# Performance work log

Hardware: AMD Instinct MI355X
Metric: run time of the kernel (lower is better)

The kernel has to match this reference:

```python
import jax, jax.numpy as jnp
import numpy as np

B, T1, T2 = 16, 1024, 1024
K1D, K2D, V1D, V2D, A = 512, 512, 256, 256, 128


def setup_inputs() -> dict:
    key = jax.random.key(0)
    ks = jax.random.split(key, 10)
    inp = {
        "k1": jax.random.normal(ks[0], (B, T1, K1D), dtype=jnp.float32),
        "k2": jax.random.normal(ks[1], (B, T2, K2D), dtype=jnp.float32),
        "v1": jax.random.normal(ks[2], (B, T1, V1D), dtype=jnp.float32),
        "v2": jax.random.normal(ks[3], (B, T2, V2D), dtype=jnp.float32),
        # Linear params (torch nn.Linear: y = x @ W.T + b)
        "W1": jax.random.normal(ks[4], (A, K1D), dtype=jnp.float32) / np.sqrt(K1D),
        "b1": jnp.zeros((A,), dtype=jnp.float32),
        "W2": jax.random.normal(ks[5], (A, K2D), dtype=jnp.float32) / np.sqrt(K2D),
        "b2": jnp.zeros((A,), dtype=jnp.float32),
        # valid lengths in [T/2, T-1] so no softmax row is entirely -inf
        "k1_lengths": jax.random.randint(ks[6], (B,), T1 // 2, T1, dtype=jnp.int32),
        "k2_lengths": jax.random.randint(ks[7], (B,), T2 // 2, T2, dtype=jnp.int32),
    }
    return inp


def reference(k1, k2, v1, v2, W1, b1, W2, b2, k1_lengths, k2_lengths):
    # projections
    q1 = jnp.einsum("bti,ai->bta", k1, W1) + b1  # [B,T1,A]
    q2 = jnp.einsum("bti,ai->bta", k2, W2) + b2  # [B,T2,A]
    # co-attention score [B,T1,T2]
    score = jnp.einsum("bia,bja->bij", q1, q2)
    # faithful mask: torch code adds 1 for rows>=l1 and 1 for cols>=l2,
    # then masks where sum == 1  -> XOR of the two pad conditions.
    row_pad = jnp.arange(T1)[None, :, None] >= k1_lengths[:, None, None]  # [B,T1,1]
    col_pad = jnp.arange(T2)[None, None, :] >= k2_lengths[:, None, None]  # [B,1,T2]
    mask = jnp.logical_xor(row_pad, col_pad)
    score = jnp.where(mask, -jnp.inf, score)
    # dual softmaxes
    w1 = jax.nn.softmax(jnp.swapaxes(score, 1, 2), axis=-1)  # [B,T2,T1]
    w2 = jax.nn.softmax(score, axis=-1)                      # [B,T1,T2]
    o1 = jnp.einsum("bji,bid->bjd", w1, v1)  # [B,T2,V1D]
    o2 = jnp.einsum("bij,bjd->bid", w2, v2)  # [B,T1,V2D]
    # note: the torch module additionally slices w1/w2/score per sample to
    # (l2,l1)/(l1,l2) ragged views; with fixed shapes we return the full
    # tensors (the valid region matches; slicing is a zero-copy view in torch).
    return (o1, o2, w1, w2, score)
```

## Files before the change

kernel.cpp:

```cpp
#include <hip/hip_runtime.h>
#include <math.h>

namespace {
constexpr int TT   = 1024;
constexpr int AD   = 128;
constexpr int KDIM = 512;
constexpr int VDIM = 256;
constexpr int NB   = 16;
constexpr size_t T2T = (size_t)TT * TT;
constexpr size_t BT  = (size_t)NB * TT;
}

#define MASK_VAL (-1.0e30f)

typedef __bf16 bf16x8 __attribute__((ext_vector_type(8)));
typedef float  f32x4  __attribute__((ext_vector_type(4)));

__device__ __forceinline__ unsigned short bf16_rne(float x) {
    unsigned int u = __builtin_bit_cast(unsigned int, x);
    u += 0x7fffu + ((u >> 16) & 1u);
    return (unsigned short)(u >> 16);
}
__device__ __forceinline__ float bf16f(unsigned short h) {
    return __builtin_bit_cast(float, ((unsigned int)h) << 16);
}
__device__ __forceinline__ void split2(float x, unsigned short& h, unsigned short& l) {
    h = bf16_rne(x);
    l = bf16_rne(x - bf16f(h));
}

__global__ __launch_bounds__(256) void prep_vt_kernel(
    const float* __restrict__ v1, const float* __restrict__ v2,
    unsigned short* __restrict__ vth, unsigned short* __restrict__ vtl)
{
    const int b     = blockIdx.x;
    const int k0    = blockIdx.y * 32;
    const int which = blockIdx.z;
    const float* vb = (which ? v1 : v2) + (size_t)b * TT * VDIM;
    const int tid = threadIdx.x;

    __shared__ float ls[32][257];
#pragma unroll
    for (int rep = 0; rep < 8; ++rep) {
        int idx = tid + rep * 256;
        int k  = idx >> 6;
        int n4 = (idx & 63) * 4;
        float4 x = *(const float4*)(vb + (size_t)(k0 + k) * VDIM + n4);
        ls[k][n4 + 0] = x.x;
        ls[k][n4 + 1] = x.y;
        ls[k][n4 + 2] = x.z;
        ls[k][n4 + 3] = x.w;
    }
    __syncthreads();

    const size_t pbase = ((size_t)(which * NB + b)) * VDIM * TT;
#pragma unroll
    for (int rep = 0; rep < 4; ++rep) {
        int idx = tid + rep * 256;
        int n  = idx >> 2;
        int sg = (idx & 3) * 8;
        unsigned short h[8], l[8];
#pragma unroll
        for (int j = 0; j < 8; ++j) {
            float x = ls[sg + j][n];
            split2(x, h[j], l[j]);
        }
        uint4 H, L;
        H.x = (unsigned)h[0] | ((unsigned)h[1] << 16);
        H.y = (unsigned)h[2] | ((unsigned)h[3] << 16);
        H.z = (unsigned)h[4] | ((unsigned)h[5] << 16);
        H.w = (unsigned)h[6] | ((unsigned)h[7] << 16);
        L.x = (unsigned)l[0] | ((unsigned)l[1] << 16);
        L.y = (unsigned)l[2] | ((unsigned)l[3] << 16);
        L.z = (unsigned)l[4] | ((unsigned)l[5] << 16);
        L.w = (unsigned)l[6] | ((unsigned)l[7] << 16);
        size_t off = pbase + (size_t)n * TT + k0 + sg;
        *(uint4*)(vth + off) = H;
        *(uint4*)(vtl + off) = L;
    }
}

__global__ __launch_bounds__(256) void qproj_mfma_kernel(
    const float* __restrict__ k1, const float* __restrict__ W1, const float* __restrict__ bias1,
    const float* __restrict__ k2, const float* __restrict__ W2, const float* __restrict__ bias2,
    unsigned short* __restrict__ q1h, unsigned short* __restrict__ q1l,
    unsigned short* __restrict__ q2h, unsigned short* __restrict__ q2l)
{
    const int proj = blockIdx.y;
    const float* __restrict__ K    = proj ? k2 : k1;
    const float* __restrict__ W    = proj ? W2 : W1;
    const float* __restrict__ bias = proj ? bias2 : bias1;
    unsigned short* __restrict__ qh = proj ? q2h : q1h;
    unsigned short* __restrict__ ql = proj ? q2l : q1l;

    const int m0 = blockIdx.x * 128;

    __shared__ alignas(16) unsigned short akh[128 * 40];
    __shared__ alignas(16) unsigned short akl[128 * 40];
    __shared__ alignas(16) unsigned short bwh[128 * 40];
    __shared__ alignas(16) unsigned short bwl[128 * 40];

    const int tid  = threadIdx.x;
    const int lane = tid & 63;
    const int wv   = tid >> 6;
    const int wm = wv >> 1, wn = wv & 1;
    const int la = lane & 15, kg = lane >> 4;

    f32x4 acc[4][4];
#pragma unroll
    for (int m = 0; m < 4; ++m)
#pragma unroll
        for (int n = 0; n < 4; ++n) acc[m][n] = (f32x4){0.f, 0.f, 0.f, 0.f};

    for (int k0 = 0; k0 < KDIM; k0 += 32) {
#pragma unroll
        for (int rep = 0; rep < 4; ++rep) {
            int idx = tid + rep * 256;
            int row = idx >> 3, c4 = (idx & 7) * 4;
            float4 x = *(const float4*)(K + (size_t)(m0 + row) * KDIM + k0 + c4);
            ushort4 H, L;
            split2(x.x, H.x, L.x);
            split2(x.y, H.y, L.y);
            split2(x.z, H.z, L.z);
            split2(x.w, H.w, L.w);
            *(ushort4*)&akh[row * 40 + c4] = H;
            *(ushort4*)&akl[row * 40 + c4] = L;
        }
#pragma unroll
        for (int rep = 0; rep < 4; ++rep) {
            int idx = tid + rep * 256;
            int row = idx >> 3, c4 = (idx & 7) * 4;
            float4 x = *(const float4*)(W + (size_t)row * KDIM + k0 + c4);
            ushort4 H, L;
            split2(x.x, H.x, L.x);
            split2(x.y, H.y, L.y);
            split2(x.z, H.z, L.z);
            split2(x.w, H.w, L.w);
            *(ushort4*)&bwh[row * 40 + c4] = H;
            *(ushort4*)&bwl[row * 40 + c4] = L;
        }
        __syncthreads();

        bf16x8 ah[4], al[4], bh[4], bl[4];
#pragma unroll
        for (int m = 0; m < 4; ++m) {
            int r = wm * 64 + m * 16 + la;
            ah[m] = *(const bf16x8*)&akh[r * 40 + kg * 8];
            al[m] = *(const bf16x8*)&akl[r * 40 + kg * 8];
        }
#pragma unroll
        for (int n = 0; n < 4; ++n) {
            int c = wn * 64 + n * 16 + la;
            bh[n] = *(const bf16x8*)&bwh[c * 40 + kg * 8];
            bl[n] = *(const bf16x8*)&bwl[c * 40 + kg * 8];
        }
#pragma unroll
        for (int m = 0; m < 4; ++m)
#pragma unroll
            for (int n = 0; n < 4; ++n) {
                acc[m][n] = __builtin_amdgcn_mfma_f32_16x16x32_bf16(ah[m], bh[n], acc[m][n], 0, 0, 0);
                acc[m][n] = __builtin_amdgcn_mfma_f32_16x16x32_bf16(ah[m], bl[n], acc[m][n], 0, 0, 0);
                acc[m][n] = __builtin_amdgcn_mfma_f32_16x16x32_bf16(al[m], bh[n], acc[m][n], 0, 0, 0);
            }
        __syncthreads();
    }

#pragma unroll
    for (int n = 0; n < 4; ++n) {
        int col = wn * 64 + n * 16 + la;
        float bv = bias[col];
#pragma unroll
        for (int m = 0; m < 4; ++m)
#pragma unroll
            for (int r = 0; r < 4; ++r) {
                int row = m0 + wm * 64 + m * 16 + kg * 4 + r;
                unsigned short h, l;
                split2(acc[m][n][r] + bv, h, l);
                qh[(size_t)row * AD + col] = h;
                ql[(size_t)row * AD + col] = l;
            }
    }
}

__global__ __launch_bounds__(256) void score_mfma_stats_kernel(
    const unsigned short* __restrict__ q1h, const unsigned short* __restrict__ q1l,
    const unsigned short* __restrict__ q2h, const unsigned short* __restrict__ q2l,
    const int* __restrict__ len1, const int* __restrict__ len2,
    float* __restrict__ score,
    float* __restrict__ prm, float* __restrict__ prs,
    float* __restrict__ pcm, float* __restrict__ pcs)
{
    const int b  = blockIdx.x;
    const int mt = blockIdx.y >> 3, nt = blockIdx.y & 7;
    const int m0 = mt * 128, n0 = nt * 128;
    const size_t qoff = (size_t)b * TT * AD;

    __shared__ alignas(16) unsigned short ath[128 * 40];
    __shared__ alignas(16) unsigned short atl[128 * 40];
    __shared__ alignas(16) unsigned short bth[128 * 40];
    __shared__ alignas(16) unsigned short btl[128 * 40];
    __shared__ float red_m[2][128];
    __shared__ float red_s[2][128];

    const int tid  = threadIdx.x;
    const int lane = tid & 63;
    const int wv   = tid >> 6;
    const int wm = wv >> 1, wn = wv & 1;
    const int la = lane & 15, kg = lane >> 4;

    f32x4 acc[4][4];
#pragma unroll
    for (int m = 0; m < 4; ++m)
#pragma unroll
        for (int n = 0; n < 4; ++n) acc[m][n] = (f32x4){0.f, 0.f, 0.f, 0.f};

    for (int k0 = 0; k0 < AD; k0 += 32) {
#pragma unroll
        for (int rep = 0; rep < 2; ++rep) {
            int idx = tid + rep * 256;
            int row = idx >> 2, sg = (idx & 3) * 8;
            *(uint4*)&ath[row * 40 + sg] = *(const uint4*)(q1h + qoff + (size_t)(m0 + row) * AD + k0 + sg);
            *(uint4*)&atl[row * 40 + sg] = *(const uint4*)(q1l + qoff + (size_t)(m0 + row) * AD + k0 + sg);
            *(uint4*)&bth[row * 40 + sg] = *(const uint4*)(q2h + qoff + (size_t)(n0 + row) * AD + k0 + sg);
            *(uint4*)&btl[row * 40 + sg] = *(const uint4*)(q2l + qoff + (size_t)(n0 + row) * AD + k0 + sg);
        }
        __syncthreads();

        bf16x8 ah[4], al[4], bh[4], bl[4];
#pragma unroll
        for (int m = 0; m < 4; ++m) {
            int r = wm * 64 + m * 16 + la;
            ah[m] = *(const bf16x8*)&ath[r * 40 + kg * 8];
            al[m] = *(const bf16x8*)&atl[r * 40 + kg * 8];
        }
#pragma unroll
        for (int n = 0; n < 4; ++n) {
            int c = wn * 64 + n * 16 + la;
            bh[n] = *(const bf16x8*)&bth[c * 40 + kg * 8];
            bl[n] = *(const bf16x8*)&btl[c * 40 + kg * 8];
        }
#pragma unroll
        for (int m = 0; m < 4; ++m)
#pragma unroll
            for (int n = 0; n < 4; ++n) {
                acc[m][n] = __builtin_amdgcn_mfma_f32_16x16x32_bf16(ah[m], bh[n], acc[m][n], 0, 0, 0);
                acc[m][n] = __builtin_amdgcn_mfma_f32_16x16x32_bf16(ah[m], bl[n], acc[m][n], 0, 0, 0);
                acc[m][n] = __builtin_amdgcn_mfma_f32_16x16x32_bf16(al[m], bh[n], acc[m][n], 0, 0, 0);
            }
        __syncthreads();
    }

    const int l1v = len1[b];
    const int l2v = len2[b];

#pragma unroll
    for (int m = 0; m < 4; ++m)
#pragma unroll
        for (int r = 0; r < 4; ++r) {
            int row = m0 + wm * 64 + m * 16 + kg * 4 + r;
            bool rp = row >= l1v;
#pragma unroll
            for (int n = 0; n < 4; ++n) {
                int col = n0 + wn * 64 + n * 16 + la;
                bool cp = col >= l2v;
                if (rp != cp) acc[m][n][r] = MASK_VAL;
            }
        }
    float* sb = score + (size_t)b * T2T;
#pragma unroll
    for (int m = 0; m < 4; ++m)
#pragma unroll
        for (int r = 0; r < 4; ++r) {
            int row = m0 + wm * 64 + m * 16 + kg * 4 + r;
#pragma unroll
            for (int n = 0; n < 4; ++n) {
                int col = n0 + wn * 64 + n * 16 + la;
                sb[(size_t)row * TT + col] = acc[m][n][r];
            }
        }

#pragma unroll
    for (int m = 0; m < 4; ++m)
#pragma unroll
        for (int r = 0; r < 4; ++r) {
            float mr = fmaxf(fmaxf(acc[m][0][r], acc[m][1][r]),
                             fmaxf(acc[m][2][r], acc[m][3][r]));
#pragma unroll
            for (int off = 1; off <= 8; off <<= 1) mr = fmaxf(mr, __shfl_xor(mr, off));
            float sr = __expf(acc[m][0][r] - mr) + __expf(acc[m][1][r] - mr) +
                       __expf(acc[m][2][r] - mr) + __expf(acc[m][3][r] - mr);
#pragma unroll
            for (int off = 1; off <= 8; off <<= 1) sr += __shfl_xor(sr, off);
            if (la == 0) {
                int rloc = wm * 64 + m * 16 + kg * 4 + r;
                red_m[wn][rloc] = mr;
                red_s[wn][rloc] = sr;
            }
        }
    __syncthreads();
    if (tid < 128) {
        float ma = red_m[0][tid], mb2 = red_m[1][tid];
        float mm = fmaxf(ma, mb2);
        float ss = red_s[0][tid] * __expf(ma - mm) + red_s[1][tid] * __expf(mb2 - mm);
        prm[(size_t)nt * BT + (size_t)b * TT + m0 + tid] = mm;
        prs[(size_t)nt * BT + (size_t)b * TT + m0 + tid] = ss;
    }
    __syncthreads();

#pragma unroll
    for (int n = 0; n < 4; ++n) {
        float mc = MASK_VAL;
#pragma unroll
        for (int m = 0; m < 4; ++m)
#pragma unroll
            for (int r = 0; r < 4; ++r) mc = fmaxf(mc, acc[m][n][r]);
#pragma unroll
        for (int off = 16; off <= 32; off <<= 1) mc = fmaxf(mc, __shfl_xor(mc, off));
        float sc = 0.f;
#pragma unroll
        for (int m = 0; m < 4; ++m)
#pragma unroll
            for (int r = 0; r < 4; ++r) sc += __expf(acc[m][n][r] - mc);
#pragma unroll
        for (int off = 16; off <= 32; off <<= 1) sc += __shfl_xor(sc, off);
        if (kg == 0) {
            int cloc = wn * 64 + n * 16 + la;
            red_m[wm][cloc] = mc;
            red_s[wm][cloc] = sc;
        }
    }
    __syncthreads();
    if (tid < 128) {
        float ma = red_m[0][tid], mb2 = red_m[1][tid];
        float mm = fmaxf(ma, mb2);
        float ss = red_s[0][tid] * __expf(ma - mm) + red_s[1][tid] * __expf(mb2 - mm);
        pcm[(size_t)mt * BT + (size_t)b * TT + n0 + tid] = mm;
        pcs[(size_t)mt * BT + (size_t)b * TT + n0 + tid] = ss;
    }
}

__global__ __launch_bounds__(256) void statcomb_kernel(
    const float* __restrict__ prm, const float* __restrict__ prs,
    const float* __restrict__ pcm, const float* __restrict__ pcs,
    float* __restrict__ rmax, float* __restrict__ rinv,
    float* __restrict__ cmax, float* __restrict__ cinv)
{
    const int id = blockIdx.x * 256 + threadIdx.x;
    const float* pm = blockIdx.y ? pcm : prm;
    const float* ps = blockIdx.y ? pcs : prs;
    float* om = blockIdx.y ? cmax : rmax;
    float* oi = blockIdx.y ? cinv : rinv;
    float nm = MASK_VAL;
#pragma unroll
    for (int c = 0; c < 8; ++c) nm = fmaxf(nm, pm[(size_t)c * BT + id]);
    float s = 0.f;
#pragma unroll
    for (int c = 0; c < 8; ++c)
        s += ps[(size_t)c * BT + id] * __expf(pm[(size_t)c * BT + id] - nm);
    om[id] = nm;
    oi[id] = 1.f / s;
}

__global__ __launch_bounds__(256) void ogemm_fused_kernel(
    const float* __restrict__ score,
    const float* __restrict__ rmax, const float* __restrict__ rinv,
    const float* __restrict__ cmax, const float* __restrict__ cinv,
    const unsigned short* __restrict__ vth, const unsigned short* __restrict__ vtl,
    float* __restrict__ w2, float* __restrict__ w1,
    float* __restrict__ o2, float* __restrict__ o1)
{
    const int b     = blockIdx.x;
    const int m0    = blockIdx.y * 64;
    const int which = blockIdx.z;
    const size_t vbase = ((size_t)(which * NB + b)) * VDIM * TT;

    const float* __restrict__ sb = score + (size_t)b * T2T;
    float* __restrict__ wout = (which ? w1 : w2) + (size_t)b * T2T;
    float* __restrict__ ob   = (which ? o1 : o2) + (size_t)b * TT * VDIM;

    __shared__ alignas(16) unsigned short awh[64 * 40];
    __shared__ alignas(16) unsigned short awl[64 * 40];
    __shared__ alignas(16) unsigned short bvh[256 * 40];
    __shared__ alignas(16) unsigned short bvl[256 * 40];
    __shared__ float st[64][33];
    __shared__ float sm_s[64], si_s[64];

    const int tid  = threadIdx.x;
    const int lane = tid & 63;
    const int wn   = tid >> 6;
    const int la = lane & 15, kg = lane >> 4;

    if (tid < 64) {
        sm_s[tid] = (which ? cmax : rmax)[(size_t)b * TT + m0 + tid];
        si_s[tid] = (which ? cinv : rinv)[(size_t)b * TT + m0 + tid];
    }
    __syncthreads();

    f32x4 acc[4][4];
#pragma unroll
    for (int m = 0; m < 4; ++m)
#pragma unroll
        for (int n = 0; n < 4; ++n) acc[m][n] = (f32x4){0.f, 0.f, 0.f, 0.f};

    for (int k0 = 0; k0 < TT; k0 += 32) {
        if (which == 0) {
#pragma unroll
            for (int rep = 0; rep < 2; ++rep) {
                int idx = tid + rep * 256;
                int row = idx >> 3, c4 = (idx & 7) * 4;
                float4 x = *(const float4*)(sb + (size_t)(m0 + row) * TT + k0 + c4);
                float mm = sm_s[row], ii = si_s[row];
                x.x = __expf(x.x - mm) * ii;
                x.y = __expf(x.y - mm) * ii;
                x.z = __expf(x.z - mm) * ii;
                x.w = __expf(x.w - mm) * ii;
                *(float4*)(wout + (size_t)(m0 + row) * TT + k0 + c4) = x;
                ushort4 H, L;
                split2(x.x, H.x, L.x);
                split2(x.y, H.y, L.y);
                split2(x.z, H.z, L.z);
                split2(x.w, H.w, L.w);
                *(ushort4*)&awh[row * 40 + c4] = H;
                *(ushort4*)&awl[row * 40 + c4] = L;
            }
        } else {
#pragma unroll
            for (int rep = 0; rep < 2; ++rep) {
                int idx = tid + rep * 256;
                int ip = idx >> 4, c4 = (idx & 15) * 4;
                float4 x = *(const float4*)(sb + (size_t)(k0 + ip) * TT + m0 + c4);
                st[c4 + 0][ip] = __expf(x.x - sm_s[c4 + 0]) * si_s[c4 + 0];
                st[c4 + 1][ip] = __expf(x.y - sm_s[c4 + 1]) * si_s[c4 + 1];
                st[c4 + 2][ip] = __expf(x.z - sm_s[c4 + 2]) * si_s[c4 + 2];
                st[c4 + 3][ip] = __expf(x.w - sm_s[c4 + 3]) * si_s[c4 + 3];
            }
            __syncthreads();
#pragma unroll
            for (int rep = 0; rep < 2; ++rep) {
                int idx = tid + rep * 256;
                int j = idx >> 3, i4 = (idx & 7) * 4;
                float v0 = st[j][i4 + 0], v1 = st[j][i4 + 1];
                float v2 = st[j][i4 + 2], v3 = st[j][i4 + 3];
                *(float4*)(wout + (size_t)(m0 + j) * TT + k0 + i4) =
                    make_float4(v0, v1, v2, v3);
                ushort4 H, L;
                split2(v0, H.x, L.x);
                split2(v1, H.y, L.y);
                split2(v2, H.z, L.z);
                split2(v3, H.w, L.w);
                *(ushort4*)&awh[j * 40 + i4] = H;
                *(ushort4*)&awl[j * 40 + i4] = L;
            }
        }
#pragma unroll
        for (int rep = 0; rep < 4; ++rep) {
            int idx = tid + rep * 256;
            int n  = idx >> 2;
            int sg = (idx & 3) * 8;
            size_t off = vbase + (size_t)n * TT + k0 + sg;
            *(uint4*)&bvh[n * 40 + sg] = *(const uint4*)(vth + off);
            *(uint4*)&bvl[n * 40 + sg] = *(const uint4*)(vtl + off);
        }
        __syncthreads();

        bf16x8 ah[4], al[4], bh[4], bl[4];
#pragma unroll
        for (int m = 0; m < 4; ++m) {
            int r = m * 16 + la;
            ah[m] = *(const bf16x8*)&awh[r * 40 + kg * 8];
            al[m] = *(const bf16x8*)&awl[r * 40 + kg * 8];
        }
#pragma unroll
        for (int n = 0; n < 4; ++n) {
            int c = wn * 64 + n * 16 + la;
            bh[n] = *(const bf16x8*)&bvh[c * 40 + kg * 8];
            bl[n] = *(const bf16x8*)&bvl[c * 40 + kg * 8];
        }
#pragma unroll
        for (int m = 0; m < 4; ++m)
#pragma unroll
            for (int n = 0; n < 4; ++n) {
                acc[m][n] = __builtin_amdgcn_mfma_f32_16x16x32_bf16(ah[m], bh[n], acc[m][n], 0, 0, 0);
                acc[m][n] = __builtin_amdgcn_mfma_f32_16x16x32_bf16(ah[m], bl[n], acc[m][n], 0, 0, 0);
                acc[m][n] = __builtin_amdgcn_mfma_f32_16x16x32_bf16(al[m], bh[n], acc[m][n], 0, 0, 0);
            }
        __syncthreads();
    }

#pragma unroll
    for (int m = 0; m < 4; ++m)
#pragma unroll
        for (int r = 0; r < 4; ++r) {
            int row = m0 + m * 16 + kg * 4 + r;
#pragma unroll
            for (int n = 0; n < 4; ++n) {
                int col = wn * 64 + n * 16 + la;
                ob[(size_t)row * VDIM + col] = acc[m][n][r];
            }
        }
}

extern "C" void kernel_launch(void* const* d_in, const int* in_sizes, int n_in,
                              void* d_out, int out_size, void* d_ws, size_t ws_size,
                              hipStream_t stream) {
    const float* k1 = (const float*)d_in[0];
    const float* k2 = (const float*)d_in[1];
    const float* v1 = (const float*)d_in[2];
    const float* v2 = (const float*)d_in[3];
    const float* W1 = (const float*)d_in[4];
    const float* b1 = (const float*)d_in[5];
    const float* W2 = (const float*)d_in[6];
    const float* b2 = (const float*)d_in[7];
    const int* len1 = (const int*)d_in[8];
    const int* len2 = (const int*)d_in[9];

    float* out = (float*)d_out;
    float* o1    = out;
    float* o2    = out + (size_t)NB * TT * VDIM;
    float* w1    = out + (size_t)2 * NB * TT * VDIM;
    float* w2    = w1 + (size_t)NB * T2T;
    float* score = w2 + (size_t)NB * T2T;

    float* ws   = (float*)d_ws;
    float* rmax = ws;
    float* rinv = rmax + BT;
    float* cmax = rinv + BT;
    float* cinv = cmax + BT;
    float* prm  = cinv + BT;
    float* prs  = prm + 8 * BT;
    float* pcm  = prs + 8 * BT;
    float* pcs  = pcm + 8 * BT;
    unsigned short* q1h = (unsigned short*)(pcs + 8 * BT);
    unsigned short* q1l = q1h + BT * AD;
    unsigned short* q2h = q1l + BT * AD;
    unsigned short* q2l = q2h + BT * AD;
    unsigned short* vth = q2l + BT * AD;
    unsigned short* vtl = vth + (size_t)32 * VDIM * TT;

    prep_vt_kernel<<<dim3(NB, TT / 32, 2), 256, 0, stream>>>(v1, v2, vth, vtl);
    qproj_mfma_kernel<<<dim3(NB * TT / 128, 2), 256, 0, stream>>>(k1, W1, b1, k2, W2, b2,
                                                                  q1h, q1l, q2h, q2l);
    score_mfma_stats_kernel<<<dim3(NB, 64), 256, 0, stream>>>(q1h, q1l, q2h, q2l,
                                                              len1, len2, score,
                                                              prm, prs, pcm, pcs);
    statcomb_kernel<<<dim3(BT / 256, 2), 256, 0, stream>>>(prm, prs, pcm, pcs,
                                                           rmax, rinv, cmax, cinv);
    ogemm_fused_kernel<<<dim3(NB, TT / 64, 2), 256, 0, stream>>>(score, rmax, rinv, cmax, cinv,
                                                                 vth, vtl, w2, w1, o2, o1);
}
```

Baseline: 195.6 us.

## Double ogemm M-tile to 128 rows with 512 threads and nontemporal stores

The fused softmax-output GEMM now handles 128 rows per block with 8 waves arranged 2x4, so each staged V tile in shared memory feeds twice as many rows and V traffic per output row is halved. The w1/w2 and o1/o2 outputs are written with nontemporal stores so these large write-once tensors bypass cache retention. The cost is half as many blocks (256), which may underfill the GPU, plus larger LDS use per block that could limit occupancy.

Result: faster. 179.5 us (-8.2%).

```diff
diff --git a/kernel.cpp b/kernel.cpp
--- a/kernel.cpp
+++ b/kernel.cpp
@@ -361,7 +361,7 @@
     oi[id] = 1.f / s;
 }
 
-__global__ __launch_bounds__(256) void ogemm_fused_kernel(
+__global__ __launch_bounds__(512) void ogemm_fused_kernel(
     const float* __restrict__ score,
     const float* __restrict__ rmax, const float* __restrict__ rinv,
     const float* __restrict__ cmax, const float* __restrict__ cinv,
@@ -370,7 +370,7 @@
     float* __restrict__ o2, float* __restrict__ o1)
 {
     const int b     = blockIdx.x;
-    const int m0    = blockIdx.y * 64;
+    const int m0    = blockIdx.y * 128;
     const int which = blockIdx.z;
     const size_t vbase = ((size_t)(which * NB + b)) * VDIM * TT;
 
@@ -378,19 +378,21 @@
     float* __restrict__ wout = (which ? w1 : w2) + (size_t)b * T2T;
     float* __restrict__ ob   = (which ? o1 : o2) + (size_t)b * TT * VDIM;
 
-    __shared__ alignas(16) unsigned short awh[64 * 40];
-    __shared__ alignas(16) unsigned short awl[64 * 40];
+    __shared__ alignas(16) unsigned short awh[128 * 40];
+    __shared__ alignas(16) unsigned short awl[128 * 40];
     __shared__ alignas(16) unsigned short bvh[256 * 40];
     __shared__ alignas(16) unsigned short bvl[256 * 40];
-    __shared__ float st[64][33];
-    __shared__ float sm_s[64], si_s[64];
+    __shared__ float st[128][33];
+    __shared__ float sm_s[128], si_s[128];
 
     const int tid  = threadIdx.x;
     const int lane = tid & 63;
-    const int wn   = tid >> 6;
+    const int wv   = tid >> 6;
+    const int wm   = wv >> 2;
+    const int wn   = wv & 3;
     const int la = lane & 15, kg = lane >> 4;
 
-    if (tid < 64) {
+    if (tid < 128) {
         sm_s[tid] = (which ? cmax : rmax)[(size_t)b * TT + m0 + tid];
         si_s[tid] = (which ? cinv : rinv)[(size_t)b * TT + m0 + tid];
     }
@@ -406,28 +408,29 @@
         if (which == 0) {
 #pragma unroll
             for (int rep = 0; rep < 2; ++rep) {
-                int idx = tid + rep * 256;
+                int idx = tid + rep * 512;
                 int row = idx >> 3, c4 = (idx & 7) * 4;
                 float4 x = *(const float4*)(sb + (size_t)(m0 + row) * TT + k0 + c4);
                 float mm = sm_s[row], ii = si_s[row];
-                x.x = __expf(x.x - mm) * ii;
-                x.y = __expf(x.y - mm) * ii;
-                x.z = __expf(x.z - mm) * ii;
-                x.w = __expf(x.w - mm) * ii;
-                *(float4*)(wout + (size_t)(m0 + row) * TT + k0 + c4) = x;
+                f32x4 wv4;
+                wv4[0] = __expf(x.x - mm) * ii;
+                wv4[1] = __expf(x.y - mm) * ii;
+                wv4[2] = __expf(x.z - mm) * ii;
+                wv4[3] = __expf(x.w - mm) * ii;
+                __builtin_nontemporal_store(wv4, (f32x4*)(wout + (size_t)(m0 + row) * TT + k0 + c4));
                 ushort4 H, L;
-                split2(x.x, H.x, L.x);
-                split2(x.y, H.y, L.y);
-                split2(x.z, H.z, L.z);
-                split2(x.w, H.w, L.w);
+                split2(wv4[0], H.x, L.x);
+                split2(wv4[1], H.y, L.y);
+                split2(wv4[2], H.z, L.z);
+                split2(wv4[3], H.w, L.w);
                 *(ushort4*)&awh[row * 40 + c4] = H;
                 *(ushort4*)&awl[row * 40 + c4] = L;
             }
         } else {
 #pragma unroll
             for (int rep = 0; rep < 2; ++rep) {
-                int idx = tid + rep * 256;
-                int ip = idx >> 4, c4 = (idx & 15) * 4;
+                int idx = tid + rep * 512;
+                int ip = idx >> 5, c4 = (idx & 31) * 4;
                 float4 x = *(const float4*)(sb + (size_t)(k0 + ip) * TT + m0 + c4);
                 st[c4 + 0][ip] = __expf(x.x - sm_s[c4 + 0]) * si_s[c4 + 0];
                 st[c4 + 1][ip] = __expf(x.y - sm_s[c4 + 1]) * si_s[c4 + 1];
@@ -437,24 +440,26 @@
             __syncthreads();
 #pragma unroll
             for (int rep = 0; rep < 2; ++rep) {
-                int idx = tid + rep * 256;
+                int idx = tid + rep * 512;
                 int j = idx >> 3, i4 = (idx & 7) * 4;
-                float v0 = st[j][i4 + 0], v1 = st[j][i4 + 1];
-                float v2 = st[j][i4 + 2], v3 = st[j][i4 + 3];
-                *(float4*)(wout + (size_t)(m0 + j) * TT + k0 + i4) =
-                    make_float4(v0, v1, v2, v3);
+                f32x4 wv4;
+                wv4[0] = st[j][i4 + 0];
+                wv4[1] = st[j][i4 + 1];
+                wv4[2] = st[j][i4 + 2];
+                wv4[3] = st[j][i4 + 3];
+                __builtin_nontemporal_store(wv4, (f32x4*)(wout + (size_t)(m0 + j) * TT + k0 + i4));
                 ushort4 H, L;
-                split2(v0, H.x, L.x);
-                split2(v1, H.y, L.y);
-                split2(v2, H.z, L.z);
-                split2(v3, H.w, L.w);
+                split2(wv4[0], H.x, L.x);
+                split2(wv4[1], H.y, L.y);
+                split2(wv4[2], H.z, L.z);
+                split2(wv4[3], H.w, L.w);
                 *(ushort4*)&awh[j * 40 + i4] = H;
                 *(ushort4*)&awl[j * 40 + i4] = L;
             }
         }
 #pragma unroll
-        for (int rep = 0; rep < 4; ++rep) {
-            int idx = tid + rep * 256;
+        for (int rep = 0; rep < 2; ++rep) {
+            int idx = tid + rep * 512;
             int n  = idx >> 2;
             int sg = (idx & 3) * 8;
             size_t off = vbase + (size_t)n * TT + k0 + sg;
@@ -466,7 +471,7 @@
         bf16x8 ah[4], al[4], bh[4], bl[4];
 #pragma unroll
         for (int m = 0; m < 4; ++m) {
-            int r = m * 16 + la;
+            int r = wm * 64 + m * 16 + la;
             ah[m] = *(const bf16x8*)&awh[r * 40 + kg * 8];
             al[m] = *(const bf16x8*)&awl[r * 40 + kg * 8];
         }
@@ -491,11 +496,11 @@
     for (int m = 0; m < 4; ++m)
 #pragma unroll
         for (int r = 0; r < 4; ++r) {
-            int row = m0 + m * 16 + kg * 4 + r;
+            int row = m0 + wm * 64 + m * 16 + kg * 4 + r;
 #pragma unroll
             for (int n = 0; n < 4; ++n) {
                 int col = wn * 64 + n * 16 + la;
-                ob[(size_t)row * VDIM + col] = acc[m][n][r];
+                __builtin_nontemporal_store(acc[m][n][r], ob + (size_t)row * VDIM + col);
             }
         }
 }
@@ -545,6 +550,6 @@
                                                               prm, prs, pcm, pcs);
     statcomb_kernel<<<dim3(BT / 256, 2), 256, 0, stream>>>(prm, prs, pcm, pcs,
                                                            rmax, rinv, cmax, cinv);
-    ogemm_fused_kernel<<<dim3(NB, TT / 64, 2), 256, 0, stream>>>(score, rmax, rinv, cmax, cinv,
-                                                                 vth, vtl, w2, w1, o2, o1);
-}
+    ogemm_fused_kernel<<<dim3(NB, TT / 128, 2), 512, 0, stream>>>(score, rmax, rinv, cmax, cinv,
+                                                                  vth, vtl, w2, w1, o2, o1);
+}
```
